# Performance work log

Measured on AMD Instinct MI355X. Metric: run time of the kernel, lower is better.

## Reference

```python
import jax, jax.numpy as jnp
import numpy as np

WIN = 8
SHIFT = 4
HEADS = 6

def _rel_pos_index(w):
    coords = np.stack(np.meshgrid(np.arange(w), np.arange(w), indexing='ij'))  # (2,w,w)
    cf = coords.reshape(2, -1)
    rel = (cf[:, :, None] - cf[:, None, :]).transpose(1, 2, 0)  # (N,N,2)
    rel[:, :, 0] += w - 1
    rel[:, :, 1] += w - 1
    rel[:, :, 0] *= 2 * w - 1
    return rel.sum(-1)  # (N,N) int

def _attn_mask(H, W, w, s):
    img = np.zeros((H, W))
    slices = (slice(0, -w), slice(-w, -s), slice(-s, None))
    cnt = 0
    for hs in slices:
        for ws in slices:
            img[hs, ws] = cnt
            cnt += 1
    mw = img.reshape(H // w, w, W // w, w).transpose(0, 2, 1, 3).reshape(-1, w * w)  # (nW,N)
    am = mw[:, None, :] - mw[:, :, None]
    return np.where(am != 0, -100.0, 0.0).astype(np.float32)  # (nW,N,N)

def _ln(z, g, b):
    mu = z.mean(-1, keepdims=True)
    var = z.var(-1, keepdims=True)
    return (z - mu) / jnp.sqrt(var + 1e-5) * g + b

def setup_inputs() -> dict:
    key = jax.random.key(0)
    ks = jax.random.split(key, 8)
    C, HID = 192, 768
    sc = lambda fan: 1.0 / np.sqrt(fan)
    return {
        'x': jax.random.normal(ks[0], (4, 256, 256, C), jnp.float32),
        'qkv_w': jax.random.normal(ks[1], (3 * C, C), jnp.float32) * sc(C),
        'qkv_b': jnp.zeros((3 * C,), jnp.float32),
        'proj_w': jax.random.normal(ks[2], (C, C), jnp.float32) * sc(C),
        'proj_b': jnp.zeros((C,), jnp.float32),
        'rpb': jax.random.normal(ks[3], (225, HEADS), jnp.float32) * 0.02,
        'n1_w': jnp.ones((C,), jnp.float32),
        'n1_b': jnp.zeros((C,), jnp.float32),
        'n2_w': jnp.ones((C,), jnp.float32),
        'n2_b': jnp.zeros((C,), jnp.float32),
        'fc1_w': jax.random.normal(ks[4], (HID, C), jnp.float32) * sc(C),
        'fc1_b': jnp.zeros((HID,), jnp.float32),
        'fc2_w': jax.random.normal(ks[5], (C, HID), jnp.float32) * sc(HID),
        'fc2_b': jnp.zeros((C,), jnp.float32),
    }

def reference(x, qkv_w, qkv_b, proj_w, proj_b, rpb, n1_w, n1_b, n2_w, n2_b, fc1_w, fc1_b, fc2_w, fc2_b):
    B, H, W, C = x.shape
    N = WIN * WIN
    hd = C // HEADS
    scale = hd ** -0.5

    shortcut = x.reshape(B, H * W, C)
    z = _ln(shortcut, n1_w, n1_b).reshape(B, H, W, C)
    z = jnp.roll(z, (-SHIFT, -SHIFT), axis=(1, 2))

    # window partition -> (B*nW, N, C)
    xw = z.reshape(B, H // WIN, WIN, W // WIN, WIN, C).transpose(0, 1, 3, 2, 4, 5).reshape(-1, N, C)
    B_ = xw.shape[0]

    qkv = (xw @ qkv_w.T + qkv_b).reshape(B_, N, 3, HEADS, hd).transpose(2, 0, 3, 1, 4)
    q, k, v = qkv[0] * scale, qkv[1], qkv[2]
    attn = jnp.einsum('bhnd,bhmd->bhnm', q, k)  # (B_,H,N,N)

    idx = _rel_pos_index(WIN)
    bias = rpb[idx.reshape(-1)].reshape(N, N, HEADS).transpose(2, 0, 1)  # (H,N,N)
    attn = attn + bias[None]

    mask = jnp.asarray(_attn_mask(H, W, WIN, SHIFT))  # (nW,N,N)
    nW = mask.shape[0]
    attn = attn.reshape(B_ // nW, nW, HEADS, N, N) + mask[None, :, None]
    attn = jax.nn.softmax(attn, axis=-1).reshape(B_, HEADS, N, N)

    out = jnp.einsum('bhnm,bhmd->bhnd', attn, v).transpose(0, 2, 1, 3).reshape(B_, N, C)
    out = out @ proj_w.T + proj_b

    # window reverse
    out = out.reshape(B, H // WIN, W // WIN, WIN, WIN, C).transpose(0, 1, 3, 2, 4, 5).reshape(B, H, W, C)
    out = jnp.roll(out, (SHIFT, SHIFT), axis=(1, 2)).reshape(B, H * W, C)

    h = shortcut + out
    m = _ln(h, n2_w, n2_b)
    m = jax.nn.gelu(m @ fc1_w.T + fc1_b, approximate=False)
    m = m @ fc2_w.T + fc2_b
    return (h + m).reshape(B, H, W, C)
```

## Files before the change

### kernel.cpp

```cpp
#include <hip/hip_runtime.h>
#include <hip/hip_bf16.h>

typedef __attribute__((ext_vector_type(8))) __bf16 bf16x8;
typedef __attribute__((ext_vector_type(4))) float f32x4;
typedef __hip_bfloat16 bf16;

#define SCALE_Q 0.17677669529663687f

#define LDSP(p) ((__attribute__((address_space(3))) unsigned int*)(unsigned long long)(p))
#define GPTR(p) ((const __attribute__((address_space(1))) unsigned int*)(unsigned long long)(p))
#define GLD16(gp, lp) __builtin_amdgcn_global_load_lds(GPTR(gp), LDSP(lp), 16, 0, 0)

__device__ inline float gelu_f(float x) {
  const float ax = fabsf(x) * 0.70710678118654752f;
  const float t = __builtin_amdgcn_rcpf(__builtin_fmaf(0.3275911f, ax, 1.0f));
  const float poly = t * __builtin_fmaf(t, __builtin_fmaf(t, __builtin_fmaf(t,
                     __builtin_fmaf(t, 1.061405429f, -1.453152027f),
                     1.421413741f), -0.284496736f), 0.254829592f);
  const float er = __builtin_fmaf(-poly, __expf(-ax * ax), 1.0f);
  return 0.5f * x * (1.0f + copysignf(er, x));
}

__global__ void cvt_kernel(const float* __restrict__ in, bf16* __restrict__ out, int n) {
  int i = blockIdx.x * 256 + threadIdx.x;
  if (i < n) out[i] = __float2bfloat16(in[i]);
}

template<bool GATHER>
__global__ __launch_bounds__(256) void ln_kernel(const float* __restrict__ in,
                                                 const float* __restrict__ gw,
                                                 const float* __restrict__ gb,
                                                 bf16* __restrict__ out) {
  const int t = blockIdx.x * 4 + (threadIdx.x >> 6);
  const int lane = threadIdx.x & 63;
  long g;
  if (GATHER) {
    const int b_ = t >> 6, n = t & 63;
    const int b = b_ >> 10, wk = b_ & 1023, wi = wk >> 5, wj = wk & 31;
    const int i_ = n >> 3, j_ = n & 7;
    const int hf = (wi * 8 + i_ + 4) & 255, wf = (wj * 8 + j_ + 4) & 255;
    g = (((long)b * 256 + hf) * 256 + wf) * 192;
  } else {
    g = (long)t * 192;
  }
  const float x0 = in[g + lane], x1 = in[g + 64 + lane], x2 = in[g + 128 + lane];
  float s = x0 + x1 + x2;
  float s2 = x0 * x0 + x1 * x1 + x2 * x2;
  #pragma unroll
  for (int m = 1; m < 64; m <<= 1) { s += __shfl_xor(s, m); s2 += __shfl_xor(s2, m); }
  const float mu = s * (1.0f / 192.0f);
  const float rstd = rsqrtf(s2 * (1.0f / 192.0f) - mu * mu + 1e-5f);
  const long o = (long)t * 192;
  out[o + lane]       = __float2bfloat16((x0 - mu) * rstd * gw[lane]       + gb[lane]);
  out[o + 64 + lane]  = __float2bfloat16((x1 - mu) * rstd * gw[lane + 64]  + gb[lane + 64]);
  out[o + 128 + lane] = __float2bfloat16((x2 - mu) * rstd * gw[lane + 128] + gb[lane + 128]);
}

template<int EPI>
__global__ __launch_bounds__(512, 4) void gemm_bt(const bf16* __restrict__ A,
                                                  const bf16* __restrict__ Bw,
                                                  const float* __restrict__ bias,
                                                  int K, void* __restrict__ outp,
                                                  const float* __restrict__ aux1,
                                                  const float* __restrict__ aux2) {
  __shared__ __align__(16) bf16 Ald[128 * 64];
  __shared__ __align__(16) bf16 Bld[192 * 64];
  const int tid = threadIdx.x;
  const int n0 = blockIdx.x * 192;
  const long m0 = (long)blockIdx.y * 128;
  const int lane = tid & 63, wid = tid >> 6;
  const int wr = (wid >> 1) * 32, wc = (wid & 1) * 96;
  const int lg = lane >> 4, lr = lane & 15;
  const int l3 = lane >> 3, l7 = lane & 7;
  const int chunk = l7 ^ l3;

  const bf16* aptr = A + (m0 + wid * 16 + l3) * (long)K + chunk * 8;
  const bf16* bptr = Bw + (n0 + wid * 24 + l3) * (long)K + chunk * 8;
  char* alds = (char*)Ald + wid * 16 * 128;
  char* blds = (char*)Bld + wid * 24 * 128;
  const long rk8 = 8 * (long)K;

  f32x4 acc[2][6];
  #pragma unroll
  for (int i = 0; i < 2; i++)
    #pragma unroll
    for (int j = 0; j < 6; j++) acc[i][j] = (f32x4){0.f, 0.f, 0.f, 0.f};

  for (int k0 = 0; k0 < K; k0 += 64) {
    GLD16(aptr + k0, alds);
    GLD16(aptr + rk8 + k0, alds + 1024);
    GLD16(bptr + k0, blds);
    GLD16(bptr + rk8 + k0, blds + 1024);
    GLD16(bptr + 2 * rk8 + k0, blds + 2048);
    __syncthreads();
    #pragma unroll
    for (int ks = 0; ks < 2; ks++) {
      bf16x8 af[2], bfr[6];
      #pragma unroll
      for (int i = 0; i < 2; i++) {
        const int row = wr + i * 16 + lr;
        af[i] = *(const bf16x8*)((const char*)Ald + row * 128 + (((ks * 4 + lg) ^ (row & 7)) * 16));
      }
      #pragma unroll
      for (int j = 0; j < 6; j++) {
        const int row = wc + j * 16 + lr;
        bfr[j] = *(const bf16x8*)((const char*)Bld + row * 128 + (((ks * 4 + lg) ^ (row & 7)) * 16));
      }
      #pragma unroll
      for (int i = 0; i < 2; i++)
        #pragma unroll
        for (int j = 0; j < 6; j++)
          acc[i][j] = __builtin_amdgcn_mfma_f32_16x16x32_bf16(af[i], bfr[j], acc[i][j], 0, 0, 0);
    }
    __syncthreads();
  }

  #pragma unroll
  for (int i = 0; i < 2; i++) {
    #pragma unroll
    for (int j = 0; j < 6; j++) {
      #pragma unroll
      for (int r = 0; r < 4; r++) {
        const long m = m0 + wr + i * 16 + lg * 4 + r;
        const int cn = n0 + wc + j * 16 + lr;
        float v = acc[i][j][r] + bias[cn];
        if (EPI == 0) {
          const long b_ = m >> 6; const int n = (int)(m & 63);
          const int which = cn / 192, rem = cn - which * 192, head = rem >> 5, d = rem & 31;
          if (which == 0) v *= SCALE_Q;
          ((bf16*)outp)[((b_ * 6 + head) * 3 + which) * 2048 + n * 32 + d] = __float2bfloat16(v);
        } else if (EPI == 1) {
          const long b_ = m >> 6; const int n = (int)(m & 63);
          const int b = (int)(b_ >> 10), wk = (int)(b_ & 1023), wi = wk >> 5, wj = wk & 31;
          const int i_ = n >> 3, j_ = n & 7;
          const int hf = (wi * 8 + i_ + 4) & 255, wf = (wj * 8 + j_ + 4) & 255;
          const long g = (((long)b * 256 + hf) * 256 + wf) * 192 + cn;
          ((float*)outp)[g] = aux1[g] + v;
        } else if (EPI == 2) {
          ((bf16*)outp)[m * 768 + cn] = __float2bfloat16(gelu_f(v));
        } else {
          ((float*)outp)[m * 192 + cn] = aux2[m * 192 + cn] + v;
        }
      }
    }
  }
}

__global__ __launch_bounds__(64) void attn_kernel(const bf16* __restrict__ qkv,
                                                  const float* __restrict__ rpb,
                                                  bf16* __restrict__ outp) {
  __shared__ __align__(16) char smem[14848];
  __shared__ float rps[225];
  const int bid = blockIdx.x;
  const int b_ = bid / 6, head = bid - b_ * 6;
  const int lane = threadIdx.x;
  const long base = ((long)b_ * 6 + head) * 3 * 2048;

  for (int t = lane; t < 225; t += 64) rps[t] = rpb[t * 6 + head];

  #pragma unroll
  for (int q = 0; q < 4; q++) {
    const int f = q * 64 + lane, row = f >> 2, c = f & 3;
    *(uint4*)(smem + row * 80 + c * 16) = *(const uint4*)(qkv + base + row * 32 + c * 8);
    *(uint4*)(smem + 5120 + row * 80 + c * 16) = *(const uint4*)(qkv + base + 2048 + row * 32 + c * 8);
  }
  {
    const bf16* vsrc = qkv + base + 4096 + lane * 32;
    bf16 vv[32];
    #pragma unroll
    for (int q = 0; q < 4; q++) *(uint4*)&vv[q * 8] = *(const uint4*)(vsrc + q * 8);
    bf16* vt = (bf16*)(smem + 10240);
    #pragma unroll
    for (int d = 0; d < 32; d++) vt[d * 72 + lane] = vv[d];
  }
  __syncthreads();

  const int lg = lane >> 4, lr = lane & 15;
  const f32x4 z4 = {0.f, 0.f, 0.f, 0.f};
  f32x4 s[4][4];
  {
    bf16x8 a[4], b[4];
    #pragma unroll
    for (int fi = 0; fi < 4; fi++)
      a[fi] = *(const bf16x8*)(smem + (fi * 16 + lr) * 80 + lg * 16);
    #pragma unroll
    for (int fj = 0; fj < 4; fj++)
      b[fj] = *(const bf16x8*)(smem + 5120 + (fj * 16 + lr) * 80 + lg * 16);
    #pragma unroll
    for (int fi = 0; fi < 4; fi++)
      #pragma unroll
      for (int fj = 0; fj < 4; fj++)
        s[fi][fj] = __builtin_amdgcn_mfma_f32_16x16x32_bf16(a[fi], b[fj], z4, 0, 0, 0);
  }

  const int wk = b_ & 1023; const int wi = wk >> 5, wj = wk & 31;
  const bool eh = (wi == 31), ew = (wj == 31);
  bf16* P = (bf16*)smem;
  #pragma unroll
  for (int fi = 0; fi < 4; fi++) {
    #pragma unroll
    for (int r = 0; r < 4; r++) {
      const int n = fi * 16 + lg * 4 + r;
      const int i1 = n >> 3, j1 = n & 7;
      const int labn = (eh ? (i1 < 4 ? 3 : 6) : 0) + (ew ? (j1 < 4 ? 1 : 2) : 0);
      float vals[4];
      #pragma unroll
      for (int fj = 0; fj < 4; fj++) {
        const int m = fj * 16 + lr;
        const int i2 = m >> 3, j2 = m & 7;
        const int labm = (eh ? (i2 < 4 ? 3 : 6) : 0) + (ew ? (j2 < 4 ? 1 : 2) : 0);
        vals[fj] = s[fi][fj][r] + rps[(i1 - i2 + 7) * 15 + (j1 - j2 + 7)]
                 + (labn != labm ? -100.0f : 0.0f);
      }
      float mx = fmaxf(fmaxf(vals[0], vals[1]), fmaxf(vals[2], vals[3]));
      #pragma unroll
      for (int msk = 1; msk < 16; msk <<= 1) mx = fmaxf(mx, __shfl_xor(mx, msk));
      float pe[4]; float sum = 0.f;
      #pragma unroll
      for (int fj = 0; fj < 4; fj++) { pe[fj] = __expf(vals[fj] - mx); sum += pe[fj]; }
      #pragma unroll
      for (int msk = 1; msk < 16; msk <<= 1) sum += __shfl_xor(sum, msk);
      const float rinv = 1.0f / sum;
      #pragma unroll
      for (int fj = 0; fj < 4; fj++)
        P[n * 72 + fj * 16 + lr] = __float2bfloat16(pe[fj] * rinv);
    }
  }
  __syncthreads();

  f32x4 o[4][2];
  #pragma unroll
  for (int fi = 0; fi < 4; fi++)
    #pragma unroll
    for (int fd = 0; fd < 2; fd++) o[fi][fd] = z4;
  const bf16* vt = (const bf16*)(smem + 10240);
  #pragma unroll
  for (int ks = 0; ks < 2; ks++) {
    bf16x8 pa[4], vb[2];
    #pragma unroll
    for (int fi = 0; fi < 4; fi++)
      pa[fi] = *(const bf16x8*)(P + (fi * 16 + lr) * 72 + ks * 32 + lg * 8);
    #pragma unroll
    for (int fd = 0; fd < 2; fd++)
      vb[fd] = *(const bf16x8*)(vt + (fd * 16 + lr) * 72 + ks * 32 + lg * 8);
    #pragma unroll
    for (int fi = 0; fi < 4; fi++)
      #pragma unroll
      for (int fd = 0; fd < 2; fd++)
        o[fi][fd] = __builtin_amdgcn_mfma_f32_16x16x32_bf16(pa[fi], vb[fd], o[fi][fd], 0, 0, 0);
  }
  #pragma unroll
  for (int fi = 0; fi < 4; fi++)
    #pragma unroll
    for (int fd = 0; fd < 2; fd++)
      #pragma unroll
      for (int r = 0; r < 4; r++) {
        const int n = fi * 16 + lg * 4 + r;
        outp[((long)b_ * 64 + n) * 192 + head * 32 + fd * 16 + lr] = __float2bfloat16(o[fi][fd][r]);
      }
}

extern "C" void kernel_launch(void* const* d_in, const int* in_sizes, int n_in,
                              void* d_out, int out_size, void* d_ws, size_t ws_size,
                              hipStream_t stream) {
  const float* x      = (const float*)d_in[0];
  const float* qkv_w  = (const float*)d_in[1];
  const float* qkv_b  = (const float*)d_in[2];
  const float* proj_w = (const float*)d_in[3];
  const float* proj_b = (const float*)d_in[4];
  const float* rpb    = (const float*)d_in[5];
  const float* n1_w   = (const float*)d_in[6];
  const float* n1_b   = (const float*)d_in[7];
  const float* n2_w   = (const float*)d_in[8];
  const float* n2_b   = (const float*)d_in[9];
  const float* fc1_w  = (const float*)d_in[10];
  const float* fc1_b  = (const float*)d_in[11];
  const float* fc2_w  = (const float*)d_in[12];
  const float* fc2_b  = (const float*)d_in[13];

  char* ws = (char*)d_ws;
  bf16* qkvw_h  = (bf16*)(ws);
  bf16* projw_h = (bf16*)(ws + 221184);
  bf16* fc1w_h  = (bf16*)(ws + 294912);
  bf16* fc2w_h  = (bf16*)(ws + 589824);
  bf16* r1      = (bf16*)(ws + (1L << 20));
  bf16* r2      = (bf16*)(ws + 101711872L);
  float* hbuf   = (float*)(ws + 504365056L);

  cvt_kernel<<<432, 256, 0, stream>>>(qkv_w, qkvw_h, 110592);
  cvt_kernel<<<144, 256, 0, stream>>>(proj_w, projw_h, 36864);
  cvt_kernel<<<576, 256, 0, stream>>>(fc1_w, fc1w_h, 147456);
  cvt_kernel<<<576, 256, 0, stream>>>(fc2_w, fc2w_h, 147456);

  ln_kernel<true><<<65536, 256, 0, stream>>>(x, n1_w, n1_b, r1);
  gemm_bt<0><<<dim3(3, 2048), 512, 0, stream>>>(r1, qkvw_h, qkv_b, 192, r2, nullptr, nullptr);
  attn_kernel<<<24576, 64, 0, stream>>>(r2, rpb, r1);
  gemm_bt<1><<<dim3(1, 2048), 512, 0, stream>>>(r1, projw_h, proj_b, 192, hbuf, x, nullptr);
  ln_kernel<false><<<65536, 256, 0, stream>>>(hbuf, n2_w, n2_b, r1);
  gemm_bt<2><<<dim3(4, 2048), 512, 0, stream>>>(r1, fc1w_h, fc1_b, 192, r2, nullptr, nullptr);
  gemm_bt<3><<<dim3(1, 2048), 512, 0, stream>>>(r2, fc2w_h, fc2_b, 768, d_out, nullptr, hbuf);
}
```

Baseline: 905.1 us.

## Fuse MLP fc1, GELU and fc2 into one kernel keeping hidden tile in LDS

Replaces the separate fc1+GELU GEMM and fc2+residual GEMM with a single kernel per 64-row tile. The GELU activation tile (64x768 bf16) stays in shared memory instead of being written to and re-read from global memory. This removes a large bf16 intermediate round trip and one launch. In exchange it uses about 120KB of LDS per block, which limits occupancy, and the fc2 weight loads are not double-buffered, so they sync on every k-step.

```diff
diff --git a/kernel.cpp b/kernel.cpp
--- a/kernel.cpp
+++ b/kernel.cpp
@@ -129,18 +129,148 @@
           const int which = cn / 192, rem = cn - which * 192, head = rem >> 5, d = rem & 31;
           if (which == 0) v *= SCALE_Q;
           ((bf16*)outp)[((b_ * 6 + head) * 3 + which) * 2048 + n * 32 + d] = __float2bfloat16(v);
-        } else if (EPI == 1) {
+        } else {
           const long b_ = m >> 6; const int n = (int)(m & 63);
           const int b = (int)(b_ >> 10), wk = (int)(b_ & 1023), wi = wk >> 5, wj = wk & 31;
           const int i_ = n >> 3, j_ = n & 7;
           const int hf = (wi * 8 + i_ + 4) & 255, wf = (wj * 8 + j_ + 4) & 255;
           const long g = (((long)b * 256 + hf) * 256 + wf) * 192 + cn;
           ((float*)outp)[g] = aux1[g] + v;
-        } else if (EPI == 2) {
-          ((bf16*)outp)[m * 768 + cn] = __float2bfloat16(gelu_f(v));
-        } else {
-          ((float*)outp)[m * 192 + cn] = aux2[m * 192 + cn] + v;
         }
+      }
+    }
+  }
+}
+
+__global__ __launch_bounds__(512, 2) void mlp_fused(const bf16* __restrict__ hln,
+                                                    const bf16* __restrict__ w1,
+                                                    const float* __restrict__ b1,
+                                                    const bf16* __restrict__ w2,
+                                                    const float* __restrict__ b2,
+                                                    const float* __restrict__ hbuf,
+                                                    float* __restrict__ outp) {
+  __shared__ __align__(16) char smem[122880];
+  char* Ab = smem;
+  char* B1 = smem + 24576;
+  char* G  = smem + 24576;
+  char* B2 = smem;
+
+  const int tid = threadIdx.x;
+  const long m0 = (long)blockIdx.x * 64;
+  const int lane = tid & 63, wid = tid >> 6;
+  const int lg = lane >> 4, lr = lane & 15;
+  const int l3 = lane >> 3, l7 = lane & 7;
+  const int chunk = l7 ^ l3;
+  const int wrr = (wid >> 2) * 32;
+  const int wc1 = (wid & 3) * 192;
+  const int wc2 = (wid & 3) * 48;
+
+  {
+    const bf16* asrc = hln + (m0 + wid * 8 + l3) * 192;
+    #pragma unroll
+    for (int q = 0; q < 3; q++)
+      GLD16(asrc + (q * 8 + chunk) * 8, Ab + q * 8192 + wid * 1024 + lane * 16);
+  }
+
+  f32x4 acc1[2][12];
+  #pragma unroll
+  for (int i = 0; i < 2; i++)
+    #pragma unroll
+    for (int j = 0; j < 12; j++) acc1[i][j] = (f32x4){0.f, 0.f, 0.f, 0.f};
+
+  const bf16* b1src = w1 + (wid * 96 + l3) * 192 + chunk * 8;
+  for (int k0 = 0; k0 < 192; k0 += 64) {
+    #pragma unroll
+    for (int q = 0; q < 12; q++)
+      GLD16(b1src + q * 8 * 192 + k0, B1 + wid * 12288 + q * 1024 + lane * 16);
+    __syncthreads();
+    const int qa = k0 >> 6;
+    #pragma unroll
+    for (int ks = 0; ks < 2; ks++) {
+      const int slot = ((ks * 4 + lg) ^ (lr & 7)) * 16;
+      bf16x8 af[2], bfr[12];
+      #pragma unroll
+      for (int i = 0; i < 2; i++)
+        af[i] = *(const bf16x8*)(Ab + qa * 8192 + (wrr + i * 16 + lr) * 128 + slot);
+      #pragma unroll
+      for (int j = 0; j < 12; j++)
+        bfr[j] = *(const bf16x8*)(B1 + (wc1 + j * 16 + lr) * 128 + slot);
+      #pragma unroll
+      for (int i = 0; i < 2; i++)
+        #pragma unroll
+        for (int j = 0; j < 12; j++)
+          acc1[i][j] = __builtin_amdgcn_mfma_f32_16x16x32_bf16(af[i], bfr[j], acc1[i][j], 0, 0, 0);
+    }
+    __syncthreads();
+  }
+
+  const bf16* b2src = w2 + (wid * 24 + l3) * 768 + chunk * 8;
+  #pragma unroll
+  for (int q = 0; q < 3; q++)
+    GLD16(b2src + q * 8 * 768, B2 + wid * 3072 + q * 1024 + lane * 16);
+
+  #pragma unroll
+  for (int j = 0; j < 12; j++) {
+    const int n = wc1 + j * 16 + lr;
+    const float bj = b1[n];
+    const int c = n >> 3;
+    #pragma unroll
+    for (int i = 0; i < 2; i++) {
+      #pragma unroll
+      for (int r = 0; r < 4; r++) {
+        const int m = wrr + i * 16 + lg * 4 + r;
+        const int slot = (c & ~7) | ((c & 7) ^ (m & 7));
+        *(unsigned short*)(G + m * 1536 + slot * 16 + (n & 7) * 2) =
+            __builtin_bit_cast(unsigned short, __float2bfloat16(gelu_f(acc1[i][j][r] + bj)));
+      }
+    }
+  }
+  __syncthreads();
+
+  f32x4 acc2[2][3];
+  #pragma unroll
+  for (int i = 0; i < 2; i++)
+    #pragma unroll
+    for (int j = 0; j < 3; j++) acc2[i][j] = (f32x4){0.f, 0.f, 0.f, 0.f};
+
+  for (int kt = 0; kt < 12; kt++) {
+    #pragma unroll
+    for (int ks = 0; ks < 2; ks++) {
+      const int slot = ((ks * 4 + lg) ^ (lr & 7)) * 16;
+      const int gc2 = kt * 8 + ks * 4 + lg;
+      const int slot2 = ((gc2 & ~7) | ((gc2 & 7) ^ (lr & 7))) * 16;
+      bf16x8 af2[2], bfr2[3];
+      #pragma unroll
+      for (int i = 0; i < 2; i++)
+        af2[i] = *(const bf16x8*)(G + (wrr + i * 16 + lr) * 1536 + slot2);
+      #pragma unroll
+      for (int j = 0; j < 3; j++)
+        bfr2[j] = *(const bf16x8*)(B2 + (wc2 + j * 16 + lr) * 128 + slot);
+      #pragma unroll
+      for (int i = 0; i < 2; i++)
+        #pragma unroll
+        for (int j = 0; j < 3; j++)
+          acc2[i][j] = __builtin_amdgcn_mfma_f32_16x16x32_bf16(af2[i], bfr2[j], acc2[i][j], 0, 0, 0);
+    }
+    __syncthreads();
+    if (kt < 11) {
+      #pragma unroll
+      for (int q = 0; q < 3; q++)
+        GLD16(b2src + q * 8 * 768 + (kt + 1) * 64, B2 + wid * 3072 + q * 1024 + lane * 16);
+      __syncthreads();
+    }
+  }
+
+  #pragma unroll
+  for (int j = 0; j < 3; j++) {
+    const int cn = wc2 + j * 16 + lr;
+    const float bj = b2[cn];
+    #pragma unroll
+    for (int i = 0; i < 2; i++) {
+      #pragma unroll
+      for (int r = 0; r < 4; r++) {
+        const long m = m0 + wrr + i * 16 + lg * 4 + r;
+        outp[m * 192 + cn] = acc2[i][j][r] + bj + hbuf[m * 192 + cn];
       }
     }
   }
@@ -297,6 +427,5 @@
   attn_kernel<<<24576, 64, 0, stream>>>(r2, rpb, r1);
   gemm_bt<1><<<dim3(1, 2048), 512, 0, stream>>>(r1, projw_h, proj_b, 192, hbuf, x, nullptr);
   ln_kernel<false><<<65536, 256, 0, stream>>>(hbuf, n2_w, n2_b, r1);
-  gemm_bt<2><<<dim3(4, 2048), 512, 0, stream>>>(r1, fc1w_h, fc1_b, 192, r2, nullptr, nullptr);
-  gemm_bt<3><<<dim3(1, 2048), 512, 0, stream>>>(r2, fc2w_h, fc2_b, 768, d_out, nullptr, hbuf);
-}
+  mlp_fused<<<4096, 512, 0, stream>>>(r1, fc1w_h, fc1_b, fc2w_h, fc2_b, hbuf, (float*)d_out);
+}
```

Result: slower. 936.8 us (+3.5%).

## Fuse fc1, GELU and fc2 into one MLP kernel keeping hidden tile in LDS

Applied to the files above, without the earlier changes.

Replaces the separate fc1+GELU and fc2 GEMM launches with a single kernel that processes 32-row tiles. It computes the 768-wide hidden activation, applies GELU and stores it as bf16 in swizzled LDS, then runs fc2 from LDS and adds the residual. This removes the global write and read of the large hidden tensor. In exchange, weights are read straight from global or cache per block without LDS staging, tiles are small, and the 60KB LDS footprint may limit occupancy.

```diff
diff --git a/kernel.cpp b/kernel.cpp
--- a/kernel.cpp
+++ b/kernel.cpp
@@ -129,19 +129,123 @@
           const int which = cn / 192, rem = cn - which * 192, head = rem >> 5, d = rem & 31;
           if (which == 0) v *= SCALE_Q;
           ((bf16*)outp)[((b_ * 6 + head) * 3 + which) * 2048 + n * 32 + d] = __float2bfloat16(v);
-        } else if (EPI == 1) {
+        } else {
           const long b_ = m >> 6; const int n = (int)(m & 63);
           const int b = (int)(b_ >> 10), wk = (int)(b_ & 1023), wi = wk >> 5, wj = wk & 31;
           const int i_ = n >> 3, j_ = n & 7;
           const int hf = (wi * 8 + i_ + 4) & 255, wf = (wj * 8 + j_ + 4) & 255;
           const long g = (((long)b * 256 + hf) * 256 + wf) * 192 + cn;
           ((float*)outp)[g] = aux1[g] + v;
-        } else if (EPI == 2) {
-          ((bf16*)outp)[m * 768 + cn] = __float2bfloat16(gelu_f(v));
-        } else {
-          ((float*)outp)[m * 192 + cn] = aux2[m * 192 + cn] + v;
         }
       }
+    }
+  }
+}
+
+__global__ __launch_bounds__(512, 4) void mlp_fused(const bf16* __restrict__ hln,
+                                                    const bf16* __restrict__ w1,
+                                                    const float* __restrict__ b1,
+                                                    const bf16* __restrict__ w2,
+                                                    const float* __restrict__ b2,
+                                                    const float* __restrict__ hbuf,
+                                                    float* __restrict__ outp) {
+  __shared__ __align__(16) char smem[61440];
+  char* Ab = smem;
+  char* G  = smem + 12288;
+
+  const int tid = threadIdx.x;
+  const long m0 = (long)blockIdx.x * 32;
+  const int lane = tid & 63, wid = tid >> 6;
+  const int lg = lane >> 4, lr = lane & 15;
+
+  {
+    const int f = wid * 64 + lane;
+    const int row = (f >> 3) & 31, q = f >> 8, slot = f & 7;
+    const int c = slot ^ (row & 7);
+    GLD16(hln + (m0 + row) * 192 + (q * 8 + c) * 8, Ab + wid * 1024 + lane * 16);
+    if (wid < 4) {
+      const int f2 = 512 + wid * 64 + lane;
+      const int row2 = (f2 >> 3) & 31, q2 = f2 >> 8, slot2 = f2 & 7;
+      const int c2 = slot2 ^ (row2 & 7);
+      GLD16(hln + (m0 + row2) * 192 + (q2 * 8 + c2) * 8, Ab + 8192 + wid * 1024 + lane * 16);
+    }
+  }
+  __syncthreads();
+
+  f32x4 acc1[2][6];
+  #pragma unroll
+  for (int i = 0; i < 2; i++)
+    #pragma unroll
+    for (int j = 0; j < 6; j++) acc1[i][j] = (f32x4){0.f, 0.f, 0.f, 0.f};
+
+  const int wc1 = wid * 96;
+  #pragma unroll
+  for (int k0 = 0; k0 < 3; k0++) {
+    #pragma unroll
+    for (int ks = 0; ks < 2; ks++) {
+      const int kk = ks * 4 + lg;
+      bf16x8 af[2], bfr[6];
+      #pragma unroll
+      for (int i = 0; i < 2; i++) {
+        const int row = i * 16 + lr;
+        af[i] = *(const bf16x8*)(Ab + k0 * 4096 + row * 128 + ((kk ^ (row & 7)) * 16));
+      }
+      #pragma unroll
+      for (int j = 0; j < 6; j++)
+        bfr[j] = *(const bf16x8*)(w1 + (wc1 + j * 16 + lr) * 192 + k0 * 64 + kk * 8);
+      #pragma unroll
+      for (int i = 0; i < 2; i++)
+        #pragma unroll
+        for (int j = 0; j < 6; j++)
+          acc1[i][j] = __builtin_amdgcn_mfma_f32_16x16x32_bf16(af[i], bfr[j], acc1[i][j], 0, 0, 0);
+    }
+  }
+
+  #pragma unroll
+  for (int j = 0; j < 6; j++) {
+    const int n = wc1 + j * 16 + lr;
+    const float bj = b1[n];
+    const int c = n >> 3;
+    #pragma unroll
+    for (int i = 0; i < 2; i++) {
+      #pragma unroll
+      for (int r = 0; r < 4; r++) {
+        const int m = i * 16 + lg * 4 + r;
+        const int slot = (c & ~7) | ((c & 7) ^ (m & 7));
+        *(unsigned short*)(G + m * 1536 + slot * 16 + (n & 7) * 2) =
+            __builtin_bit_cast(unsigned short, __float2bfloat16(gelu_f(acc1[i][j][r] + bj)));
+      }
+    }
+  }
+  __syncthreads();
+
+  const int wt = wid >> 2, wn = wid & 3;
+  f32x4 acc2[3];
+  #pragma unroll
+  for (int j = 0; j < 3; j++) acc2[j] = (f32x4){0.f, 0.f, 0.f, 0.f};
+
+  const int grow = wt * 16 + lr;
+  for (int kt = 0; kt < 24; kt++) {
+    const int c2 = kt * 4 + lg;
+    const int slot2 = (c2 & ~7) | ((c2 & 7) ^ (grow & 7));
+    const bf16x8 af2 = *(const bf16x8*)(G + grow * 1536 + slot2 * 16);
+    bf16x8 bfr2[3];
+    #pragma unroll
+    for (int j = 0; j < 3; j++)
+      bfr2[j] = *(const bf16x8*)(w2 + (wn * 48 + j * 16 + lr) * 768 + kt * 32 + lg * 8);
+    #pragma unroll
+    for (int j = 0; j < 3; j++)
+      acc2[j] = __builtin_amdgcn_mfma_f32_16x16x32_bf16(af2, bfr2[j], acc2[j], 0, 0, 0);
+  }
+
+  #pragma unroll
+  for (int j = 0; j < 3; j++) {
+    const int cn = wn * 48 + j * 16 + lr;
+    const float bj = b2[cn];
+    #pragma unroll
+    for (int r = 0; r < 4; r++) {
+      const long m = m0 + wt * 16 + lg * 4 + r;
+      outp[m * 192 + cn] = acc2[j][r] + bj + hbuf[m * 192 + cn];
     }
   }
 }
@@ -297,6 +401,5 @@
   attn_kernel<<<24576, 64, 0, stream>>>(r2, rpb, r1);
   gemm_bt<1><<<dim3(1, 2048), 512, 0, stream>>>(r1, projw_h, proj_b, 192, hbuf, x, nullptr);
   ln_kernel<false><<<65536, 256, 0, stream>>>(hbuf, n2_w, n2_b, r1);
-  gemm_bt<2><<<dim3(4, 2048), 512, 0, stream>>>(r1, fc1w_h, fc1_b, 192, r2, nullptr, nullptr);
-  gemm_bt<3><<<dim3(1, 2048), 512, 0, stream>>>(r2, fc2w_h, fc2_b, 768, d_out, nullptr, hbuf);
-}
+  mlp_fused<<<8192, 512, 0, stream>>>(r1, fc1w_h, fc1_b, fc2w_h, fc2_b, hbuf, (float*)d_out);
+}
```

After: 1.311 ms. 1.45x slower.
